# Kernel tuning notes

Measured on AMD Instinct MI355X. Metric: run time of the kernel, lower is better.

Reference implementation:

```python
import jax, jax.numpy as jnp
import numpy as np

N = 131072   # total nodes
E = 262144   # directed edges (avg degree 2, molecular graphs)
G = 4096     # number of graphs in the batch
H = 64       # hidden_dim


def _linear_init(key, fan_in, fan_out):
    # torch.nn.Linear default: U(-1/sqrt(fan_in), 1/sqrt(fan_in))
    s = 1.0 / np.sqrt(fan_in)
    kw, kb = jax.random.split(key)
    W = jax.random.uniform(kw, (fan_in, fan_out), jnp.float32, -s, s)
    b = jax.random.uniform(kb, (fan_out,), jnp.float32, -s, s)
    return W, b


def setup_inputs() -> dict:
    key = jax.random.key(0)
    ks = jax.random.split(key, 8)
    d = {}
    d["x"] = jax.random.normal(ks[0], (N, 1), jnp.float32)
    d["edge_index"] = jax.random.randint(ks[1], (2, E), 0, N, jnp.int32)
    d["batch"] = jnp.sort(jax.random.randint(ks[2], (N,), 0, G, jnp.int32))
    d["W1"], d["b1"] = _linear_init(ks[3], 1, H)          # GCNConv(1, 64)
    d["W2"], d["b2"] = _linear_init(ks[4], H, 2 * H)       # GCNConv(64, 128)
    d["W3"], d["b3"] = _linear_init(ks[5], 2 * H, 4 * H)   # GCNConv(128, 256)
    d["fc1_W"], d["fc1_b"] = _linear_init(ks[6], 4 * H, 128)
    d["fc2_W"], d["fc2_b"] = _linear_init(ks[7], 128, 12)
    return d


def gcn_conv(x, W, b, src, dst):
    """PyG GCNConv: D^-1/2 (A + I) D^-1/2 (x W) + b, self-loops added."""
    h = x @ W                                                   # [N, out]
    deg = jax.ops.segment_sum(jnp.ones(E, jnp.float32), dst, num_segments=N) + 1.0
    dinv = jax.lax.rsqrt(deg)                                   # [N]
    coef = dinv[src] * dinv[dst]                                # [E]
    agg = jax.ops.segment_sum(h[src] * coef[:, None], dst, num_segments=N)
    agg = agg + h * (dinv * dinv)[:, None]                      # self-loop term: h_i / deg_i
    return agg + b


def reference(x, edge_index, batch, W1, b1, W2, b2, W3, b3, fc1_W, fc1_b, fc2_W, fc2_b):
    src, dst = edge_index[0], edge_index[1]
    h = jax.nn.relu(gcn_conv(x, W1, b1, src, dst))
    h = jax.nn.relu(gcn_conv(h, W2, b2, src, dst))
    h = gcn_conv(h, W3, b3, src, dst)                            # [N, 256]
    # global_mean_pool over batch ids
    sums = jax.ops.segment_sum(h, batch, num_segments=G)         # [G, 256]
    cnts = jax.ops.segment_sum(jnp.ones(N, jnp.float32), batch, num_segments=G)
    g = sums / jnp.maximum(cnts, 1.0)[:, None]
    g = jax.nn.relu(g @ fc1_W + fc1_b)
    return g @ fc2_W + fc2_b                                     # [G, 12]
```

## Files before the change

### kernel.cpp

```cpp
#include <hip/hip_runtime.h>

#define NN 131072
#define EE 262144
#define GG 4096

__global__ void k_zero(int4* __restrict__ p, int n4) {
    int i = blockIdx.x * 256 + threadIdx.x;
    if (i < n4) p[i] = make_int4(0, 0, 0, 0);
}

__global__ void k_count(const int* __restrict__ dst, int* __restrict__ indeg) {
    int e = blockIdx.x * 256 + threadIdx.x;
    if (e < EE) atomicAdd(&indeg[dst[e]], 1);
}

__global__ __launch_bounds__(256) void k_scan_a(const int* __restrict__ indeg,
                                                int* __restrict__ bsum,
                                                float* __restrict__ dinv,
                                                const int* __restrict__ batch,
                                                int* __restrict__ gstart) {
    __shared__ int red[256];
    int tid = threadIdx.x;
    int gid = blockIdx.x * 256 + tid;
    int v = indeg[gid];
    dinv[gid] = rsqrtf((float)v + 1.0f);
    red[tid] = v;
    {
        int b1v = batch[gid];
        int b0v = (gid == 0) ? -1 : batch[gid - 1];
        for (int g = b0v + 1; g <= b1v; ++g) gstart[g] = gid;
        if (gid == NN - 1)
            for (int g = b1v + 1; g <= GG; ++g) gstart[g] = NN;
    }
    __syncthreads();
#pragma unroll
    for (int off = 128; off > 0; off >>= 1) {
        if (tid < off) red[tid] += red[tid + off];
        __syncthreads();
    }
    if (tid == 0) bsum[blockIdx.x] = red[0];
}

__global__ __launch_bounds__(512) void k_scan_b(const int* __restrict__ bsum,
                                                int* __restrict__ boff) {
    __shared__ int ps[512];
    int tid = threadIdx.x;
    ps[tid] = bsum[tid];
    __syncthreads();
    for (int off = 1; off < 512; off <<= 1) {
        int v = (tid >= off) ? ps[tid - off] : 0;
        __syncthreads();
        ps[tid] += v;
        __syncthreads();
    }
    boff[tid] = (tid > 0) ? ps[tid - 1] : 0;
    if (tid == 511) boff[512] = ps[511];
}

__global__ __launch_bounds__(256) void k_scan_c(const int* __restrict__ indeg,
                                                const int* __restrict__ boff,
                                                int* __restrict__ rowptr,
                                                int* __restrict__ cursor) {
    __shared__ int ps[256];
    int tid = threadIdx.x;
    int gid = blockIdx.x * 256 + tid;
    int v = indeg[gid];
    ps[tid] = v;
    __syncthreads();
    for (int off = 1; off < 256; off <<= 1) {
        int t = (tid >= off) ? ps[tid - off] : 0;
        __syncthreads();
        ps[tid] += t;
        __syncthreads();
    }
    int excl = boff[blockIdx.x] + ps[tid] - v;
    rowptr[gid] = excl;
    cursor[gid] = excl;
    if (gid == NN - 1) rowptr[NN] = boff[512];
}

__global__ void k_fill_edges(const int* __restrict__ src, const int* __restrict__ dst,
                             const float* __restrict__ dinv,
                             int* __restrict__ cursor, int* __restrict__ ecol,
                             float* __restrict__ ecoef) {
    int e = blockIdx.x * 256 + threadIdx.x;
    if (e < EE) {
        int d = dst[e], s = src[e];
        int slot = atomicAdd(&cursor[d], 1);
        ecol[slot] = s;
        ecoef[slot] = dinv[d] * dinv[s];
    }
}

__global__ void k_z(const float* __restrict__ x, const float* __restrict__ dinv,
                    const int* __restrict__ rowptr, const int* __restrict__ ecol,
                    const float* __restrict__ ecoef, float* __restrict__ z) {
    int i = blockIdx.x * 256 + threadIdx.x;
    if (i < NN) {
        float di = dinv[i];
        float s = x[i] * di * di;
        int e0 = rowptr[i], e1 = rowptr[i + 1];
        for (int e = e0; e < e1; ++e) s += ecoef[e] * x[ecol[e]];
        z[i] = s;
    }
}

__global__ __launch_bounds__(256) void k_gemm2u(const float* __restrict__ z,
                                                const float* __restrict__ dinv,
                                                const int* __restrict__ rowptr,
                                                const int* __restrict__ ecol,
                                                const float* __restrict__ ecoef,
                                                const float* __restrict__ W1,
                                                const float* __restrict__ b1,
                                                const float* __restrict__ W2,
                                                const float* __restrict__ b2,
                                                float* __restrict__ r) {
    __shared__ float At[64][65];
    __shared__ float Wt[32][128];
    __shared__ float w1s[64], b1s[64];

    int tid = threadIdx.x;
    int i0 = blockIdx.x * 64;

    if (tid < 64) { w1s[tid] = W1[tid]; b1s[tid] = b1[tid]; }
    __syncthreads();

    {
        int n = tid >> 2;
        int k0 = (tid & 3) * 16;
        int i = i0 + n;
        float zi = z[i], di = dinv[i];
        float d2 = di * di;
        float uacc[16];
#pragma unroll
        for (int j = 0; j < 16; ++j)
            uacc[j] = d2 * fmaxf(zi * w1s[k0 + j] + b1s[k0 + j], 0.f);
        int e0 = rowptr[i], e1 = rowptr[i + 1];
        for (int e = e0; e < e1; ++e) {
            float w = ecoef[e];
            float zs = z[ecol[e]];
#pragma unroll
            for (int j = 0; j < 16; ++j)
                uacc[j] += w * fmaxf(zs * w1s[k0 + j] + b1s[k0 + j], 0.f);
        }
#pragma unroll
        for (int j = 0; j < 16; ++j) At[n][k0 + j] = uacc[j];
    }

    int colg = tid & 15;
    int rowg = tid >> 4;
    float acc[4][8];
#pragma unroll
    for (int rr = 0; rr < 4; ++rr)
#pragma unroll
        for (int c = 0; c < 8; ++c) acc[rr][c] = 0.0f;

    for (int kc = 0; kc < 2; ++kc) {
        if (kc) __syncthreads();
        {
            int c4 = tid & 31, kk0 = tid >> 5;
#pragma unroll
            for (int p = 0; p < 4; ++p) {
                int kk = kk0 + p * 8;
                *(float4*)&Wt[kk][c4 * 4] =
                    *(const float4*)&W2[(size_t)(kc * 32 + kk) * 128 + c4 * 4];
            }
        }
        __syncthreads();
#pragma unroll 4
        for (int kk = 0; kk < 32; ++kk) {
            float a[4];
#pragma unroll
            for (int rr = 0; rr < 4; ++rr) a[rr] = At[rowg * 4 + rr][kc * 32 + kk];
            const float4 w0 = *(const float4*)&Wt[kk][colg * 4];
            const float4 w1 = *(const float4*)&Wt[kk][64 + colg * 4];
            float w[8] = {w0.x, w0.y, w0.z, w0.w, w1.x, w1.y, w1.z, w1.w};
#pragma unroll
            for (int rr = 0; rr < 4; ++rr)
#pragma unroll
                for (int c = 0; c < 8; ++c) acc[rr][c] += a[rr] * w[c];
        }
    }

#pragma unroll
    for (int rr = 0; rr < 4; ++rr) {
        int i = i0 + rowg * 4 + rr;
#pragma unroll
        for (int h = 0; h < 2; ++h) {
            int j = h * 64 + colg * 4;
            const float4 b = *(const float4*)&b2[j];
            float4 v;
            v.x = fmaxf(acc[rr][h * 4 + 0] + b.x, 0.f);
            v.y = fmaxf(acc[rr][h * 4 + 1] + b.y, 0.f);
            v.z = fmaxf(acc[rr][h * 4 + 2] + b.z, 0.f);
            v.w = fmaxf(acc[rr][h * 4 + 3] + b.w, 0.f);
            *(float4*)&r[(size_t)i * 128 + j] = v;
        }
    }
}

template <int K, int OUTW, bool RELU_OUT, bool GUARD>
__global__ __launch_bounds__(256) void k_gemm(const float* __restrict__ A,
                                              const float* __restrict__ W,
                                              const float* __restrict__ bias,
                                              const float* __restrict__ cntf,
                                              float* __restrict__ C) {
    __shared__ float At[64][68];
    __shared__ float Wt[64][128];

    int tid  = threadIdx.x;
    int colg = tid & 15;
    int rowg = tid >> 4;
    int i0 = blockIdx.x * 64;
    int j0 = blockIdx.y * 128;

    float acc[4][8];
#pragma unroll
    for (int r = 0; r < 4; ++r)
#pragma unroll
        for (int c = 0; c < 8; ++c) acc[r][c] = 0.0f;

    for (int k0 = 0; k0 < K; k0 += 64) {
        __syncthreads();
        {
            int k4 = tid & 15, r0 = tid >> 4;
#pragma unroll
            for (int p = 0; p < 4; ++p) {
                int r = r0 + p * 16;
                *(float4*)&At[r][k4 * 4] =
                    *(const float4*)&A[(size_t)(i0 + r) * K + k0 + k4 * 4];
            }
        }
        {
            int c4 = tid & 31, kk0 = tid >> 5;
#pragma unroll
            for (int p = 0; p < 8; ++p) {
                int kk = kk0 + p * 8;
                *(float4*)&Wt[kk][c4 * 4] =
                    *(const float4*)&W[(size_t)(k0 + kk) * OUTW + j0 + c4 * 4];
            }
        }
        __syncthreads();
#pragma unroll 4
        for (int kk = 0; kk < 64; ++kk) {
            float a[4];
#pragma unroll
            for (int r = 0; r < 4; ++r) a[r] = At[rowg * 4 + r][kk];
            const float4 w0 = *(const float4*)&Wt[kk][colg * 4];
            const float4 w1 = *(const float4*)&Wt[kk][64 + colg * 4];
            float w[8] = {w0.x, w0.y, w0.z, w0.w, w1.x, w1.y, w1.z, w1.w};
#pragma unroll
            for (int r = 0; r < 4; ++r)
#pragma unroll
                for (int c = 0; c < 8; ++c) acc[r][c] += a[r] * w[c];
        }
    }

#pragma unroll
    for (int r = 0; r < 4; ++r) {
        int i = i0 + rowg * 4 + r;
        float flag = 1.0f;
        if (GUARD) flag = (cntf[i] > 0.0f) ? 1.0f : 0.0f;
#pragma unroll
        for (int h = 0; h < 2; ++h) {
            int j = j0 + h * 64 + colg * 4;
            const float4 b = *(const float4*)&bias[j];
            float4 v;
            v.x = acc[r][h * 4 + 0] + b.x * flag;
            v.y = acc[r][h * 4 + 1] + b.y * flag;
            v.z = acc[r][h * 4 + 2] + b.z * flag;
            v.w = acc[r][h * 4 + 3] + b.w * flag;
            if (RELU_OUT) {
                v.x = fmaxf(v.x, 0.f); v.y = fmaxf(v.y, 0.f);
                v.z = fmaxf(v.z, 0.f); v.w = fmaxf(v.w, 0.f);
            }
            *(float4*)&C[(size_t)i * OUTW + j] = v;
        }
    }
}

__global__ __launch_bounds__(256) void k_fc12(const float* __restrict__ A,
                                              const float* __restrict__ W,
                                              const float* __restrict__ bias,
                                              const float* __restrict__ fc2W,
                                              const float* __restrict__ fc2b,
                                              float* __restrict__ out) {
    __shared__ float At[64][68];
    __shared__ float Wt[64][128];

    int tid  = threadIdx.x;
    int colg = tid & 15;
    int rowg = tid >> 4;
    int i0 = blockIdx.x * 64;

    float acc[4][8];
#pragma unroll
    for (int r = 0; r < 4; ++r)
#pragma unroll
        for (int c = 0; c < 8; ++c) acc[r][c] = 0.0f;

    for (int k0 = 0; k0 < 256; k0 += 64) {
        __syncthreads();
        {
            int k4 = tid & 15, r0 = tid >> 4;
#pragma unroll
            for (int p = 0; p < 4; ++p) {
                int r = r0 + p * 16;
                *(float4*)&At[r][k4 * 4] =
                    *(const float4*)&A[(size_t)(i0 + r) * 256 + k0 + k4 * 4];
            }
        }
        {
            int c4 = tid & 31, kk0 = tid >> 5;
#pragma unroll
            for (int p = 0; p < 8; ++p) {
                int kk = kk0 + p * 8;
                *(float4*)&Wt[kk][c4 * 4] =
                    *(const float4*)&W[(size_t)(k0 + kk) * 128 + c4 * 4];
            }
        }
        __syncthreads();
#pragma unroll 4
        for (int kk = 0; kk < 64; ++kk) {
            float a[4];
#pragma unroll
            for (int r = 0; r < 4; ++r) a[r] = At[rowg * 4 + r][kk];
            const float4 w0 = *(const float4*)&Wt[kk][colg * 4];
            const float4 w1 = *(const float4*)&Wt[kk][64 + colg * 4];
            float w[8] = {w0.x, w0.y, w0.z, w0.w, w1.x, w1.y, w1.z, w1.w};
#pragma unroll
            for (int r = 0; r < 4; ++r)
#pragma unroll
                for (int c = 0; c < 8; ++c) acc[r][c] += a[r] * w[c];
        }
    }
    __syncthreads();
    float* g1s = &Wt[0][0];
    float* w2s = &At[0][0];
    for (int idx = tid; idx < 128 * 12; idx += 256) w2s[idx] = fc2W[idx];

#pragma unroll
    for (int r = 0; r < 4; ++r) {
        int row = rowg * 4 + r;
#pragma unroll
        for (int h = 0; h < 2; ++h) {
            int j = h * 64 + colg * 4;
            const float4 b = *(const float4*)&bias[j];
            float4 v;
            v.x = fmaxf(acc[r][h * 4 + 0] + b.x, 0.f);
            v.y = fmaxf(acc[r][h * 4 + 1] + b.y, 0.f);
            v.z = fmaxf(acc[r][h * 4 + 2] + b.z, 0.f);
            v.w = fmaxf(acc[r][h * 4 + 3] + b.w, 0.f);
            *(float4*)&g1s[row * 128 + j] = v;
        }
    }
    __syncthreads();
    for (int idx = tid; idx < 64 * 12; idx += 256) {
        int row = idx / 12, col = idx % 12;
        float o = fc2b[col];
        const float* gr = &g1s[row * 128];
        for (int k = 0; k < 128; ++k) o += gr[k] * w2s[k * 12 + col];
        out[(size_t)(i0 + row) * 12 + col] = o;
    }
}

__global__ __launch_bounds__(256) void k_pool(const float* __restrict__ r,
                                              const float* __restrict__ dinv,
                                              const int* __restrict__ rowptr,
                                              const int* __restrict__ ecol,
                                              const float* __restrict__ ecoef,
                                              const int* __restrict__ gstart,
                                              float* __restrict__ Y,
                                              float* __restrict__ cntf) {
    int g = blockIdx.x, tid = threadIdx.x;
    int lo = gstart[g], hi = gstart[g + 1];
    int cnt = hi - lo;

    int lane = tid & 31, ty = tid >> 5;
    int c = lane * 4;
    float4 acc = {0.f, 0.f, 0.f, 0.f};

    int i = lo + ty;
    for (; i + 8 < hi; i += 16) {
        float d0 = dinv[i], d1 = dinv[i + 8];
        const float4 v0 = *(const float4*)&r[(size_t)i * 128 + c];
        const float4 v1 = *(const float4*)&r[(size_t)(i + 8) * 128 + c];
        float w0 = d0 * d0, w1 = d1 * d1;
        acc.x += v0.x * w0 + v1.x * w1;
        acc.y += v0.y * w0 + v1.y * w1;
        acc.z += v0.z * w0 + v1.z * w1;
        acc.w += v0.w * w0 + v1.w * w1;
    }
    for (; i < hi; i += 8) {
        float di = dinv[i], d2 = di * di;
        const float4 v = *(const float4*)&r[(size_t)i * 128 + c];
        acc.x += v.x * d2; acc.y += v.y * d2; acc.z += v.z * d2; acc.w += v.w * d2;
    }

    int e0 = rowptr[lo], e1 = rowptr[hi];
    int e = e0 + ty;
    for (; e + 24 < e1; e += 32) {
        int s0 = ecol[e], s1 = ecol[e + 8], s2 = ecol[e + 16], s3 = ecol[e + 24];
        float w0 = ecoef[e], w1 = ecoef[e + 8], w2 = ecoef[e + 16], w3 = ecoef[e + 24];
        const float4 v0 = *(const float4*)&r[(size_t)s0 * 128 + c];
        const float4 v1 = *(const float4*)&r[(size_t)s1 * 128 + c];
        const float4 v2 = *(const float4*)&r[(size_t)s2 * 128 + c];
        const float4 v3 = *(const float4*)&r[(size_t)s3 * 128 + c];
        acc.x += v0.x * w0 + v1.x * w1 + v2.x * w2 + v3.x * w3;
        acc.y += v0.y * w0 + v1.y * w1 + v2.y * w2 + v3.y * w3;
        acc.z += v0.z * w0 + v1.z * w1 + v2.z * w2 + v3.z * w3;
        acc.w += v0.w * w0 + v1.w * w1 + v2.w * w2 + v3.w * w3;
    }
    for (; e < e1; e += 8) {
        int s = ecol[e];
        float w = ecoef[e];
        const float4 v = *(const float4*)&r[(size_t)s * 128 + c];
        acc.x += v.x * w; acc.y += v.y * w; acc.z += v.z * w; acc.w += v.w * w;
    }

    __shared__ float red[8][128];
    *(float4*)&red[ty][c] = acc;
    __syncthreads();
    if (tid < 128) {
        float s = 0.0f;
#pragma unroll
        for (int t = 0; t < 8; ++t) s += red[t][tid];
        float inv = (cnt > 0) ? 1.0f / (float)cnt : 0.0f;
        Y[(size_t)g * 128 + tid] = s * inv;
    }
    if (tid == 0) cntf[g] = (float)cnt;
}

extern "C" void kernel_launch(void* const* d_in, const int* in_sizes, int n_in,
                              void* d_out, int out_size, void* d_ws, size_t ws_size,
                              hipStream_t stream) {
    const float* x     = (const float*)d_in[0];
    const int*   ei    = (const int*)d_in[1];
    const int*   batch = (const int*)d_in[2];
    const float* W1    = (const float*)d_in[3];
    const float* b1    = (const float*)d_in[4];
    const float* W2    = (const float*)d_in[5];
    const float* b2    = (const float*)d_in[6];
    const float* W3    = (const float*)d_in[7];
    const float* b3    = (const float*)d_in[8];
    const float* fc1W  = (const float*)d_in[9];
    const float* fc1b  = (const float*)d_in[10];
    const float* fc2W  = (const float*)d_in[11];
    const float* fc2b  = (const float*)d_in[12];
    float* out = (float*)d_out;

    const int* srcp = ei;
    const int* dstp = ei + EE;

    float* r      = (float*)d_ws;
    float* Y      = r + (size_t)NN * 128;
    float* pooled = Y + (size_t)GG * 128;
    float* cntf   = pooled + (size_t)GG * 256;
    float* dinv   = cntf + GG;
    float* zbuf   = dinv + NN;
    float* ecoef  = zbuf + NN;
    int* indeg  = (int*)(ecoef + EE);
    int* rowptr = indeg + NN;
    int* cursor = rowptr + NN + 4;
    int* ecol   = cursor + NN;
    int* bsum   = ecol + EE;
    int* boff   = bsum + 512;
    int* gstart = boff + 516;

    k_zero<<<NN / 4 / 256, 256, 0, stream>>>((int4*)indeg, NN / 4);
    k_count<<<EE / 256, 256, 0, stream>>>(dstp, indeg);
    k_scan_a<<<NN / 256, 256, 0, stream>>>(indeg, bsum, dinv, batch, gstart);
    k_scan_b<<<1, 512, 0, stream>>>(bsum, boff);
    k_scan_c<<<NN / 256, 256, 0, stream>>>(indeg, boff, rowptr, cursor);
    k_fill_edges<<<EE / 256, 256, 0, stream>>>(srcp, dstp, dinv, cursor, ecol, ecoef);

    k_z<<<NN / 256, 256, 0, stream>>>(x, dinv, rowptr, ecol, ecoef, zbuf);

    k_gemm2u<<<NN / 64, 256, 0, stream>>>(zbuf, dinv, rowptr, ecol, ecoef,
                                          W1, b1, W2, b2, r);

    k_pool<<<GG, 256, 0, stream>>>(r, dinv, rowptr, ecol, ecoef, gstart, Y, cntf);

    k_gemm<128, 256, false, true><<<dim3(GG / 64, 2), 256, 0, stream>>>(
        Y, W3, b3, cntf, pooled);
    k_fc12<<<GG / 64, 256, 0, stream>>>(pooled, fc1W, fc1b, fc2W, fc2b, out);
}
```

Before: 148.0 us.

## Replace layer-2 GEMM with piecewise-linear breakpoint tables and store activations in fp16

Layer 1 has a scalar input, so relu(z*W1+b1)@W2 is piecewise linear in z with breakpoints at -b1/W1. A tiny kernel sorts the breakpoints and builds prefix tables A[m], B[m]. Each node then gets a bucket index by binary search, and the layer-2 aggregation becomes a table lookup plus a few FMAs per edge instead of a 64x128 GEMM. The layer-2 output is also stored in fp16, halving the gather traffic in the pooling kernel at the cost of reduced precision.

```diff
diff --git a/kernel.cpp b/kernel.cpp
--- a/kernel.cpp
+++ b/kernel.cpp
@@ -1,4 +1,5 @@
 #include <hip/hip_runtime.h>
+#include <hip/hip_fp16.h>
 
 #define NN 131072
 #define EE 262144
@@ -92,111 +93,178 @@
     }
 }
 
+__global__ __launch_bounds__(128) void k_table(const float* __restrict__ W1,
+                                               const float* __restrict__ b1,
+                                               const float* __restrict__ W2,
+                                               float* __restrict__ Atab,
+                                               float* __restrict__ Btab,
+                                               float* __restrict__ tss) {
+    __shared__ float tsh[64], w1sh[64], b1sh[64];
+    __shared__ int perm[64];
+    int tid = threadIdx.x;
+    if (tid < 64) {
+        float w = W1[tid], b = b1[tid];
+        w1sh[tid] = w; b1sh[tid] = b;
+        tsh[tid] = (w != 0.f) ? (-b / w) : 1e30f;
+    }
+    __syncthreads();
+    if (tid < 64) {
+        float t = tsh[tid];
+        int rank = 0;
+        for (int j = 0; j < 64; ++j) {
+            float tj = tsh[j];
+            rank += (tj < t) || (tj == t && j < tid);
+        }
+        perm[rank] = tid;
+    }
+    __syncthreads();
+    if (tid < 64) tss[tid] = tsh[perm[tid]];
+
+    int c = tid;
+    float A = 0.f, B = 0.f;
+    for (int k = 0; k < 64; ++k) {
+        float w = w1sh[k], b = b1sh[k];
+        float w2 = W2[k * 128 + c];
+        if (w < 0.f || (w == 0.f && b > 0.f)) { A += w * w2; B += b * w2; }
+    }
+    Atab[c] = A; Btab[c] = B;
+    for (int m = 1; m <= 64; ++m) {
+        int k = perm[m - 1];
+        float w = w1sh[k], b = b1sh[k];
+        float w2 = W2[k * 128 + c];
+        if (w > 0.f)      { A += w * w2; B += b * w2; }
+        else if (w < 0.f) { A -= w * w2; B -= b * w2; }
+        Atab[m * 128 + c] = A; Btab[m * 128 + c] = B;
+    }
+}
+
 __global__ void k_z(const float* __restrict__ x, const float* __restrict__ dinv,
                     const int* __restrict__ rowptr, const int* __restrict__ ecol,
-                    const float* __restrict__ ecoef, float* __restrict__ z) {
-    int i = blockIdx.x * 256 + threadIdx.x;
+                    const float* __restrict__ ecoef, const float* __restrict__ tss,
+                    float2* __restrict__ zm) {
+    __shared__ float tsh[64];
+    int tid = threadIdx.x;
+    if (tid < 64) tsh[tid] = tss[tid];
+    __syncthreads();
+    int i = blockIdx.x * 256 + tid;
     if (i < NN) {
         float di = dinv[i];
         float s = x[i] * di * di;
         int e0 = rowptr[i], e1 = rowptr[i + 1];
         for (int e = e0; e < e1; ++e) s += ecoef[e] * x[ecol[e]];
-        z[i] = s;
-    }
-}
-
-__global__ __launch_bounds__(256) void k_gemm2u(const float* __restrict__ z,
-                                                const float* __restrict__ dinv,
-                                                const int* __restrict__ rowptr,
-                                                const int* __restrict__ ecol,
-                                                const float* __restrict__ ecoef,
-                                                const float* __restrict__ W1,
-                                                const float* __restrict__ b1,
-                                                const float* __restrict__ W2,
-                                                const float* __restrict__ b2,
-                                                float* __restrict__ r) {
-    __shared__ float At[64][65];
-    __shared__ float Wt[32][128];
-    __shared__ float w1s[64], b1s[64];
-
-    int tid = threadIdx.x;
-    int i0 = blockIdx.x * 64;
-
-    if (tid < 64) { w1s[tid] = W1[tid]; b1s[tid] = b1[tid]; }
-    __syncthreads();
-
-    {
-        int n = tid >> 2;
-        int k0 = (tid & 3) * 16;
-        int i = i0 + n;
-        float zi = z[i], di = dinv[i];
-        float d2 = di * di;
-        float uacc[16];
-#pragma unroll
-        for (int j = 0; j < 16; ++j)
-            uacc[j] = d2 * fmaxf(zi * w1s[k0 + j] + b1s[k0 + j], 0.f);
-        int e0 = rowptr[i], e1 = rowptr[i + 1];
-        for (int e = e0; e < e1; ++e) {
-            float w = ecoef[e];
-            float zs = z[ecol[e]];
-#pragma unroll
-            for (int j = 0; j < 16; ++j)
-                uacc[j] += w * fmaxf(zs * w1s[k0 + j] + b1s[k0 + j], 0.f);
-        }
-#pragma unroll
-        for (int j = 0; j < 16; ++j) At[n][k0 + j] = uacc[j];
-    }
-
-    int colg = tid & 15;
-    int rowg = tid >> 4;
-    float acc[4][8];
-#pragma unroll
-    for (int rr = 0; rr < 4; ++rr)
-#pragma unroll
-        for (int c = 0; c < 8; ++c) acc[rr][c] = 0.0f;
-
-    for (int kc = 0; kc < 2; ++kc) {
-        if (kc) __syncthreads();
-        {
-            int c4 = tid & 31, kk0 = tid >> 5;
-#pragma unroll
-            for (int p = 0; p < 4; ++p) {
-                int kk = kk0 + p * 8;
-                *(float4*)&Wt[kk][c4 * 4] =
-                    *(const float4*)&W2[(size_t)(kc * 32 + kk) * 128 + c4 * 4];
-            }
-        }
-        __syncthreads();
-#pragma unroll 4
-        for (int kk = 0; kk < 32; ++kk) {
-            float a[4];
-#pragma unroll
-            for (int rr = 0; rr < 4; ++rr) a[rr] = At[rowg * 4 + rr][kc * 32 + kk];
-            const float4 w0 = *(const float4*)&Wt[kk][colg * 4];
-            const float4 w1 = *(const float4*)&Wt[kk][64 + colg * 4];
-            float w[8] = {w0.x, w0.y, w0.z, w0.w, w1.x, w1.y, w1.z, w1.w};
-#pragma unroll
-            for (int rr = 0; rr < 4; ++rr)
-#pragma unroll
-                for (int c = 0; c < 8; ++c) acc[rr][c] += a[rr] * w[c];
-        }
-    }
-
-#pragma unroll
-    for (int rr = 0; rr < 4; ++rr) {
-        int i = i0 + rowg * 4 + rr;
-#pragma unroll
-        for (int h = 0; h < 2; ++h) {
-            int j = h * 64 + colg * 4;
-            const float4 b = *(const float4*)&b2[j];
-            float4 v;
-            v.x = fmaxf(acc[rr][h * 4 + 0] + b.x, 0.f);
-            v.y = fmaxf(acc[rr][h * 4 + 1] + b.y, 0.f);
-            v.z = fmaxf(acc[rr][h * 4 + 2] + b.z, 0.f);
-            v.w = fmaxf(acc[rr][h * 4 + 3] + b.w, 0.f);
-            *(float4*)&r[(size_t)i * 128 + j] = v;
-        }
-    }
+        int lo = 0, hi = 64;
+        while (lo < hi) { int mid = (lo + hi) >> 1; if (tsh[mid] <= s) lo = mid + 1; else hi = mid; }
+        zm[i] = make_float2(s, __int_as_float(lo));
+    }
+}
+
+__global__ __launch_bounds__(256) void k_r(const float2* __restrict__ zm,
+                                           const float* __restrict__ dinv,
+                                           const int* __restrict__ rowptr,
+                                           const int* __restrict__ ecol,
+                                           const float* __restrict__ ecoef,
+                                           const float* __restrict__ Atab,
+                                           const float* __restrict__ Btab,
+                                           const float* __restrict__ b2,
+                                           __half* __restrict__ rh) {
+    int tid = threadIdx.x;
+    int i = blockIdx.x * 8 + (tid >> 5);
+    int c = (tid & 31) * 4;
+    float2 zi = zm[i];
+    float di = dinv[i];
+    float w0 = di * di;
+    int mi = __float_as_int(zi.y);
+    const float4 Av = *(const float4*)&Atab[mi * 128 + c];
+    const float4 Bv = *(const float4*)&Btab[mi * 128 + c];
+    float wz = w0 * zi.x;
+    float4 acc;
+    acc.x = wz * Av.x + w0 * Bv.x;
+    acc.y = wz * Av.y + w0 * Bv.y;
+    acc.z = wz * Av.z + w0 * Bv.z;
+    acc.w = wz * Av.w + w0 * Bv.w;
+    int e0 = rowptr[i], e1 = rowptr[i + 1];
+    for (int e = e0; e < e1; ++e) {
+        int s = ecol[e];
+        float w = ecoef[e];
+        float2 zs = zm[s];
+        int ms = __float_as_int(zs.y);
+        const float4 A2 = *(const float4*)&Atab[ms * 128 + c];
+        const float4 B2 = *(const float4*)&Btab[ms * 128 + c];
+        float wz2 = w * zs.x;
+        acc.x += wz2 * A2.x + w * B2.x;
+        acc.y += wz2 * A2.y + w * B2.y;
+        acc.z += wz2 * A2.z + w * B2.z;
+        acc.w += wz2 * A2.w + w * B2.w;
+    }
+    const float4 bb = *(const float4*)&b2[c];
+    __half2 p0 = __floats2half2_rn(fmaxf(acc.x + bb.x, 0.f), fmaxf(acc.y + bb.y, 0.f));
+    __half2 p1 = __floats2half2_rn(fmaxf(acc.z + bb.z, 0.f), fmaxf(acc.w + bb.w, 0.f));
+    union { __half2 h[2]; float2 f; } u;
+    u.h[0] = p0; u.h[1] = p1;
+    *(float2*)&rh[(size_t)i * 128 + c] = u.f;
+}
+
+__device__ inline float4 ldr4(const __half* __restrict__ rh, size_t idx) {
+    union { float2 f; __half2 h[2]; } u;
+    u.f = *(const float2*)&rh[idx];
+    float2 lo = __half22float2(u.h[0]);
+    float2 hi = __half22float2(u.h[1]);
+    return make_float4(lo.x, lo.y, hi.x, hi.y);
+}
+
+__global__ __launch_bounds__(256) void k_pool(const __half* __restrict__ rh,
+                                              const float* __restrict__ dinv,
+                                              const int* __restrict__ rowptr,
+                                              const int* __restrict__ ecol,
+                                              const float* __restrict__ ecoef,
+                                              const int* __restrict__ gstart,
+                                              float* __restrict__ Y,
+                                              float* __restrict__ cntf) {
+    int g = blockIdx.x, tid = threadIdx.x;
+    int lo = gstart[g], hi = gstart[g + 1];
+    int cnt = hi - lo;
+
+    int lane = tid & 31, ty = tid >> 5;
+    int c = lane * 4;
+    float4 acc = {0.f, 0.f, 0.f, 0.f};
+
+    for (int i = lo + ty; i < hi; i += 8) {
+        float di = dinv[i], d2 = di * di;
+        const float4 v = ldr4(rh, (size_t)i * 128 + c);
+        acc.x += v.x * d2; acc.y += v.y * d2; acc.z += v.z * d2; acc.w += v.w * d2;
+    }
+    int e0 = rowptr[lo], e1 = rowptr[hi];
+    int e = e0 + ty;
+    for (; e + 24 < e1; e += 32) {
+        int s0 = ecol[e], s1 = ecol[e + 8], s2 = ecol[e + 16], s3 = ecol[e + 24];
+        float w0 = ecoef[e], w1 = ecoef[e + 8], w2 = ecoef[e + 16], w3 = ecoef[e + 24];
+        const float4 v0 = ldr4(rh, (size_t)s0 * 128 + c);
+        const float4 v1 = ldr4(rh, (size_t)s1 * 128 + c);
+        const float4 v2 = ldr4(rh, (size_t)s2 * 128 + c);
+        const float4 v3 = ldr4(rh, (size_t)s3 * 128 + c);
+        acc.x += v0.x * w0 + v1.x * w1 + v2.x * w2 + v3.x * w3;
+        acc.y += v0.y * w0 + v1.y * w1 + v2.y * w2 + v3.y * w3;
+        acc.z += v0.z * w0 + v1.z * w1 + v2.z * w2 + v3.z * w3;
+        acc.w += v0.w * w0 + v1.w * w1 + v2.w * w2 + v3.w * w3;
+    }
+    for (; e < e1; e += 8) {
+        int s = ecol[e];
+        float w = ecoef[e];
+        const float4 v = ldr4(rh, (size_t)s * 128 + c);
+        acc.x += v.x * w; acc.y += v.y * w; acc.z += v.z * w; acc.w += v.w * w;
+    }
+
+    __shared__ float red[8][128];
+    *(float4*)&red[ty][c] = acc;
+    __syncthreads();
+    if (tid < 128) {
+        float s = 0.0f;
+#pragma unroll
+        for (int t = 0; t < 8; ++t) s += red[t][tid];
+        float inv = (cnt > 0) ? 1.0f / (float)cnt : 0.0f;
+        Y[(size_t)g * 128 + tid] = s * inv;
+    }
+    if (tid == 0) cntf[g] = (float)cnt;
 }
 
 template <int K, int OUTW, bool RELU_OUT, bool GUARD>
@@ -362,73 +430,6 @@
         for (int k = 0; k < 128; ++k) o += gr[k] * w2s[k * 12 + col];
         out[(size_t)(i0 + row) * 12 + col] = o;
     }
-}
-
-__global__ __launch_bounds__(256) void k_pool(const float* __restrict__ r,
-                                              const float* __restrict__ dinv,
-                                              const int* __restrict__ rowptr,
-                                              const int* __restrict__ ecol,
-                                              const float* __restrict__ ecoef,
-                                              const int* __restrict__ gstart,
-                                              float* __restrict__ Y,
-                                              float* __restrict__ cntf) {
-    int g = blockIdx.x, tid = threadIdx.x;
-    int lo = gstart[g], hi = gstart[g + 1];
-    int cnt = hi - lo;
-
-    int lane = tid & 31, ty = tid >> 5;
-    int c = lane * 4;
-    float4 acc = {0.f, 0.f, 0.f, 0.f};
-
-    int i = lo + ty;
-    for (; i + 8 < hi; i += 16) {
-        float d0 = dinv[i], d1 = dinv[i + 8];
-        const float4 v0 = *(const float4*)&r[(size_t)i * 128 + c];
-        const float4 v1 = *(const float4*)&r[(size_t)(i + 8) * 128 + c];
-        float w0 = d0 * d0, w1 = d1 * d1;
-        acc.x += v0.x * w0 + v1.x * w1;
-        acc.y += v0.y * w0 + v1.y * w1;
-        acc.z += v0.z * w0 + v1.z * w1;
-        acc.w += v0.w * w0 + v1.w * w1;
-    }
-    for (; i < hi; i += 8) {
-        float di = dinv[i], d2 = di * di;
-        const float4 v = *(const float4*)&r[(size_t)i * 128 + c];
-        acc.x += v.x * d2; acc.y += v.y * d2; acc.z += v.z * d2; acc.w += v.w * d2;
-    }
-
-    int e0 = rowptr[lo], e1 = rowptr[hi];
-    int e = e0 + ty;
-    for (; e + 24 < e1; e += 32) {
-        int s0 = ecol[e], s1 = ecol[e + 8], s2 = ecol[e + 16], s3 = ecol[e + 24];
-        float w0 = ecoef[e], w1 = ecoef[e + 8], w2 = ecoef[e + 16], w3 = ecoef[e + 24];
-        const float4 v0 = *(const float4*)&r[(size_t)s0 * 128 + c];
-        const float4 v1 = *(const float4*)&r[(size_t)s1 * 128 + c];
-        const float4 v2 = *(const float4*)&r[(size_t)s2 * 128 + c];
-        const float4 v3 = *(const float4*)&r[(size_t)s3 * 128 + c];
-        acc.x += v0.x * w0 + v1.x * w1 + v2.x * w2 + v3.x * w3;
-        acc.y += v0.y * w0 + v1.y * w1 + v2.y * w2 + v3.y * w3;
-        acc.z += v0.z * w0 + v1.z * w1 + v2.z * w2 + v3.z * w3;
-        acc.w += v0.w * w0 + v1.w * w1 + v2.w * w2 + v3.w * w3;
-    }
-    for (; e < e1; e += 8) {
-        int s = ecol[e];
-        float w = ecoef[e];
-        const float4 v = *(const float4*)&r[(size_t)s * 128 + c];
-        acc.x += v.x * w; acc.y += v.y * w; acc.z += v.z * w; acc.w += v.w * w;
-    }
-
-    __shared__ float red[8][128];
-    *(float4*)&red[ty][c] = acc;
-    __syncthreads();
-    if (tid < 128) {
-        float s = 0.0f;
-#pragma unroll
-        for (int t = 0; t < 8; ++t) s += red[t][tid];
-        float inv = (cnt > 0) ? 1.0f / (float)cnt : 0.0f;
-        Y[(size_t)g * 128 + tid] = s * inv;
-    }
-    if (tid == 0) cntf[g] = (float)cnt;
 }
 
 extern "C" void kernel_launch(void* const* d_in, const int* in_sizes, int n_in,
@@ -452,14 +453,18 @@
     const int* srcp = ei;
     const int* dstp = ei + EE;
 
-    float* r      = (float*)d_ws;
-    float* Y      = r + (size_t)NN * 128;
+    float* ws     = (float*)d_ws;
+    __half* rh    = (__half*)ws;
+    float* Y      = ws + (size_t)NN * 64;
     float* pooled = Y + (size_t)GG * 128;
     float* cntf   = pooled + (size_t)GG * 256;
     float* dinv   = cntf + GG;
-    float* zbuf   = dinv + NN;
-    float* ecoef  = zbuf + NN;
-    int* indeg  = (int*)(ecoef + EE);
+    float2* zm    = (float2*)(dinv + NN);
+    float* ecoef  = (float*)(zm + NN);
+    float* Atab   = ecoef + EE;
+    float* Btab   = Atab + 65 * 128;
+    float* tss    = Btab + 65 * 128;
+    int* indeg  = (int*)(tss + 64);
     int* rowptr = indeg + NN;
     int* cursor = rowptr + NN + 4;
     int* ecol   = cursor + NN;
@@ -474,12 +479,13 @@
     k_scan_c<<<NN / 256, 256, 0, stream>>>(indeg, boff, rowptr, cursor);
     k_fill_edges<<<EE / 256, 256, 0, stream>>>(srcp, dstp, dinv, cursor, ecol, ecoef);
 
-    k_z<<<NN / 256, 256, 0, stream>>>(x, dinv, rowptr, ecol, ecoef, zbuf);
-
-    k_gemm2u<<<NN / 64, 256, 0, stream>>>(zbuf, dinv, rowptr, ecol, ecoef,
-                                          W1, b1, W2, b2, r);
-
-    k_pool<<<GG, 256, 0, stream>>>(r, dinv, rowptr, ecol, ecoef, gstart, Y, cntf);
+    k_table<<<1, 128, 0, stream>>>(W1, b1, W2, Atab, Btab, tss);
+
+    k_z<<<NN / 256, 256, 0, stream>>>(x, dinv, rowptr, ecol, ecoef, tss, zm);
+
+    k_r<<<NN / 8, 256, 0, stream>>>(zm, dinv, rowptr, ecol, ecoef, Atab, Btab, b2, rh);
+
+    k_pool<<<GG, 256, 0, stream>>>(rh, dinv, rowptr, ecol, ecoef, gstart, Y, cntf);
 
     k_gemm<128, 256, false, true><<<dim3(GG / 64, 2), 256, 0, stream>>>(
         Y, W3, b3, cntf, pooled);
```

Result: slower. 165.3 us (+11.7%).
